# Kernel optimization log

Measured on AMD Instinct MI355X. Metric: run time of the kernel, lower is better.

The kernel has to match this reference:

```python
import jax, jax.numpy as jnp
from jax import lax
import numpy as np

N, D, H, ENT = 32768, 16, 128, 50000


def setup_inputs() -> dict:
    key = jax.random.key(0)
    ks = jax.random.split(key, 10)
    s = 0.05  # weight scale to keep tanh/sigmoid in active range
    return {
        "ent_table": jax.random.normal(ks[0], (ENT, H), jnp.float32) * s,
        "op_table": jax.random.normal(ks[1], (5, H), jnp.float32) * s,
        "non_table": jax.random.normal(ks[2], (1, H), jnp.float32) * s,
        "Wm": jax.random.normal(ks[3], (H, 3 * H), jnp.float32) * s,
        "bm": jnp.zeros((H,), jnp.float32),
        "Wg": jax.random.normal(ks[4], (H, 3 * H), jnp.float32) * s,
        "bg": jnp.zeros((H,), jnp.float32),
        "ops_idx": jax.random.randint(ks[5], (N, D), 0, 4, jnp.int32),
        "ents_idx": jax.random.randint(ks[6], (N, D + 1), 0, ENT, jnp.int32),
        "left_idx": jax.random.randint(ks[7], (N,), 0, ENT, jnp.int32),
    }


def reference(ent_table, op_table, non_table, Wm, bm, Wg, bg, ops_idx, ents_idx, left_idx):
    # Merge module (dropout in eval mode = identity):
    #   tanh(Linear([node, t1, t2])) * sigmoid(Linear_g([node, t1, t2]))
    def merge(node, t1, t2):
        x = jnp.concatenate([node, t1, t2], axis=-1)  # [N, 3H]
        return jnp.tanh(x @ Wm.T + bm) * jax.nn.sigmoid(x @ Wg.T + bg)

    op_e = op_table[ops_idx]        # [N, D, H]
    ent_e = ent_table[ents_idx]     # [N, D+1, H]

    # Right-leaning prefix tree: acc starts at deepest entity, merge upward.
    acc0 = ent_e[:, -1]             # [N, H]
    # scan over depth, from innermost (i = D-1) to outermost (i = 0)
    xs = (jnp.flip(op_e, axis=1).transpose(1, 0, 2),          # [D, N, H]
          jnp.flip(ent_e[:, :-1], axis=1).transpose(1, 0, 2))  # [D, N, H]

    def step(acc, inp):
        o, e = inp
        return merge(o, e, acc), None

    acc, _ = lax.scan(step, acc0, xs)

    eq_e = jnp.broadcast_to(op_table[4], acc.shape)  # '=' embedding, [N, H]
    left_e = ent_table[left_idx]                     # [N, H]
    score = merge(eq_e, left_e, acc)                 # [N, H]

    # all_score = cat(per-formula scores, non_embed)  -> [N+1, H]
    return jnp.concatenate([score, non_table], axis=0)
```

## Files before the change

kernel.cpp:

```cpp
#include <hip/hip_runtime.h>
#include <hip/hip_bf16.h>

#define NROWS 32768
#define HH 128
#define ENTN 50000

typedef _Float16 f16x8 __attribute__((ext_vector_type(8)));
typedef __fp16 fp16x2 __attribute__((ext_vector_type(2)));
typedef float f32x4 __attribute__((ext_vector_type(4)));

#define OFF_PEB 0
#define OFF_EB  25600000
#define OFF_WF  38400000
#define OFF_PEF (OFF_WF + 65536)
#define OFF_PO  (OFF_PEF + 65536)

#define KM 2.8853901f
#define KG (-1.4426950f)
#define RSTR 272
#define HALF (32 * RSTR)

#if defined(__has_builtin)
#if __has_builtin(__builtin_amdgcn_exp2f)
#define FEXP2(x) __builtin_amdgcn_exp2f(x)
#endif
#endif
#ifndef FEXP2
__device__ __forceinline__ float __fexp2_asm(float x) {
    float r; asm("v_exp_f32 %0, %1" : "=v"(r) : "v"(x)); return r;
}
#define FEXP2(x) __fexp2_asm(x)
#endif

__device__ __forceinline__ unsigned pk2(float a, float b) {
    fp16x2 h = __builtin_amdgcn_cvt_pkrtz(a, b);
    unsigned u; __builtin_memcpy(&u, &h, 4); return u;
}
__device__ __forceinline__ float h2f(unsigned short s) {
    _Float16 h; __builtin_memcpy(&h, &s, 2); return (float)h;
}

__global__ void prep_kernel(const float* __restrict__ ent_table,
                            const float* __restrict__ op_table,
                            const float* __restrict__ non_table,
                            const float* __restrict__ Wm, const float* __restrict__ bm,
                            const float* __restrict__ Wg, const float* __restrict__ bg,
                            char* __restrict__ ws, float* __restrict__ out) {
    int idx = blockIdx.x * blockDim.x + threadIdx.x;
    if (idx < 800000) {
        _Float16* EB = (_Float16*)(ws + OFF_EB);
        int base = idx * 8;
        const float4* s = (const float4*)(ent_table + base);
        float4 v0 = s[0], v1 = s[1];
        float xv[8] = {v0.x, v0.y, v0.z, v0.w, v1.x, v1.y, v1.z, v1.w};
        _Float16 h8[8];
        #pragma unroll
        for (int j = 0; j < 8; ++j) h8[j] = (_Float16)xv[j];
        *(f16x8*)(EB + base) = *(f16x8*)h8;
    } else if (idx < 832768) {
        int e = idx - 800000;
        int jj = e & 7, l = (e >> 3) & 63, kt = (e >> 9) & 3, jb = e >> 11;
        int j = jb * 16 + (l & 15);
        int c = j >> 1, p = j & 1;
        int k = kt * 32 + (l >> 4) * 8 + jj;
        const float* Wrow = p ? (Wg + (size_t)c * 384) : (Wm + (size_t)c * 384);
        ((_Float16*)(ws + OFF_WF))[e] = (_Float16)Wrow[256 + k];
    } else if (idx < 865536) {
        int e = idx - 832768;
        int jj = e & 7, l = (e >> 3) & 63, kt = (e >> 9) & 3, jb = e >> 11;
        int j = jb * 16 + (l & 15);
        int c = j >> 1, p = j & 1;
        int k = kt * 32 + (l >> 4) * 8 + jj;
        const float* Wrow = p ? (Wg + (size_t)c * 384) : (Wm + (size_t)c * 384);
        ((_Float16*)(ws + OFF_PEF))[e] = (_Float16)Wrow[128 + k];
    } else if (idx < 866816) {
        int e = idx - 865536;
        int o = e >> 8, jj = e & 255;
        int c = jj >> 1, p = jj & 1;
        const float* Wrow = p ? (Wg + (size_t)c * 384) : (Wm + (size_t)c * 384);
        float s = p ? bg[c] : bm[c];
        for (int i = 0; i < 128; ++i) s += op_table[o * HH + i] * Wrow[i];
        s *= (p ? KG : KM);
        ((float*)(ws + OFF_PO))[o * 260 + (c >> 1) * 4 + 2 * (c & 1) + p] = s;
    } else if (idx < 866944) {
        int j = idx - 866816;
        out[(size_t)NROWS * HH + j] = non_table[j];
    }
}

__global__ __launch_bounds__(256, 4)
void pe_kernel(char* __restrict__ ws) {
    const char* EBc = ws + OFF_EB;
    const f16x8* PEF = (const f16x8*)(ws + OFF_PEF);
    unsigned* PEB = (unsigned*)(ws + OFF_PEB);
    int tid = threadIdx.x, w = tid >> 6, l = tid & 63, lr = l & 15, lg = (l >> 4) & 3;
    int e0 = blockIdx.x * 32;

    f16x8 WB[4][4];
    #pragma unroll
    for (int u = 0; u < 4; ++u)
        #pragma unroll
        for (int kt = 0; kt < 4; ++kt)
            WB[u][kt] = PEF[((4 * w + u) * 4 + kt) * 64 + l];

    f32x4 C[2][4];
    #pragma unroll
    for (int rt = 0; rt < 2; ++rt)
        #pragma unroll
        for (int u = 0; u < 4; ++u) C[rt][u] = (f32x4){0.f, 0.f, 0.f, 0.f};

    #pragma unroll
    for (int kt = 0; kt < 4; ++kt) {
        #pragma unroll
        for (int rt = 0; rt < 2; ++rt) {
            int e = e0 + rt * 16 + lr;
            if (e >= ENTN) e = ENTN - 1;
            f16x8 A = *(const f16x8*)(EBc + (size_t)e * 256 + kt * 64 + lg * 16);
            #pragma unroll
            for (int u = 0; u < 4; ++u)
                C[rt][u] = __builtin_amdgcn_mfma_f32_16x16x32_f16(WB[u][kt], A, C[rt][u], 0, 0, 0);
        }
    }
    #pragma unroll
    for (int rt = 0; rt < 2; ++rt) {
        int e = e0 + rt * 16 + lr;
        if (e < ENTN) {
            #pragma unroll
            for (int u = 0; u < 4; ++u) {
                uint2 st;
                st.x = pk2(C[rt][u][0] * KM, C[rt][u][1] * KG);
                st.y = pk2(C[rt][u][2] * KM, C[rt][u][3] * KG);
                *(uint2*)(PEB + (size_t)e * HH + (4 * w + u) * 8 + 2 * lg) = st;
            }
        }
    }
}

__global__ __launch_bounds__(1024, 8)
void chain_kernel(const float* __restrict__ ent_table,
                  const int* __restrict__ ops_idx,
                  const int* __restrict__ ents_idx,
                  const int* __restrict__ left_idx,
                  const char* __restrict__ ws, float* __restrict__ out) {
    __shared__ char Abuf[2 * HALF];
    __shared__ unsigned eo[32 * 17];
    __shared__ float po_s[5 * 260];

    const char* PEBc = ws + OFF_PEB;
    const f16x8* WF2p = (const f16x8*)(ws + OFF_WF);
    const float* POg = (const float*)(ws + OFF_PO);

    int tid = threadIdx.x;
    int jb = tid >> 6, l = tid & 63, lr = l & 15, lg = (l >> 4) & 3;
    int row0 = blockIdx.x * 32;
    int c1 = jb * 8 + 2 * lg;

    if (tid < 544) {
        int r = tid / 17, t = tid - r * 17;
        unsigned e, o;
        if (t < 16) {
            e = ents_idx[(row0 + r) * 17 + 15 - t];
            o = ops_idx[(row0 + r) * 16 + 15 - t];
        } else {
            e = left_idx[row0 + r];
            o = 4;
        }
        eo[tid] = (e << 9) | o;
    }
    for (int i = tid; i < 1300; i += 1024) po_s[i] = POg[i];

    f16x8 WH[4];
    #pragma unroll
    for (int kt = 0; kt < 4; ++kt)
        WH[kt] = WF2p[(jb * 4 + kt) * 64 + l];

    {
        int r = tid >> 5, sub = tid & 31;
        int e = ents_idx[(row0 + r) * 17 + 16];
        float4 v = *(const float4*)(ent_table + (size_t)e * HH + sub * 4);
        uint2 d;
        d.x = pk2(v.x, v.y);
        d.y = pk2(v.z, v.w);
        *(uint2*)(Abuf + r * RSTR + sub * 8) = d;
    }
    __syncthreads();

    int rb = lr * RSTR + lg * 16;
    int wb = lr * RSTR + jb * 16 + 4 * lg;
    const char* pebBase = PEBc + c1 * 4;
    const float* poBase = po_s + (4 * jb + lg) * 4;
    const unsigned* eoB = eo + lr * 17;

    const f32x4 K4 = (f32x4){KM, KG, KM, KG};

    unsigned va = eoB[0], vb = eoB[272];
    uint2 pea = *(const uint2*)(pebBase + (va & 0xFFFFFE00u));
    uint2 peb = *(const uint2*)(pebBase + (vb & 0xFFFFFE00u));

#define DO_STEP(T, RD, WR, FINAL)                                               \
    {                                                                           \
        uint2 npea, npeb; unsigned nva = 0, nvb = 0;                            \
        if (!(FINAL)) {                                                         \
            nva = eoB[(T) + 1];                                                 \
            nvb = eoB[272 + (T) + 1];                                           \
            npea = *(const uint2*)(pebBase + (nva & 0xFFFFFE00u));              \
            npeb = *(const uint2*)(pebBase + (nvb & 0xFFFFFE00u));              \
        }                                                                       \
        f32x4 poa = *(const f32x4*)(poBase + (va & 7u) * 260);                  \
        f32x4 pob = *(const f32x4*)(poBase + (vb & 7u) * 260);                  \
        f32x4 C0 = (f32x4){0.f, 0.f, 0.f, 0.f};                                 \
        f32x4 C1 = (f32x4){0.f, 0.f, 0.f, 0.f};                                 \
        _Pragma("unroll")                                                       \
        for (int kt = 0; kt < 4; ++kt) {                                        \
            f16x8 A0 = *(const f16x8*)(Abuf + rb + (RD) + kt * 64);             \
            f16x8 A1 = *(const f16x8*)(Abuf + rb + (RD) + 16 * RSTR + kt * 64); \
            C0 = __builtin_amdgcn_mfma_f32_16x16x32_f16(WH[kt], A0, C0, 0, 0, 0); \
            C1 = __builtin_amdgcn_mfma_f32_16x16x32_f16(WH[kt], A1, C1, 0, 0, 0); \
        }                                                                       \
        _Pragma("unroll")                                                       \
        for (int rt = 0; rt < 2; ++rt) {                                        \
            uint2 pe = rt ? peb : pea;                                          \
            f32x4 po = rt ? pob : poa;                                          \
            f32x4 z = rt ? C1 : C0;                                             \
            f32x4 pef;                                                          \
            pef[0] = h2f((unsigned short)pe.x);                                 \
            pef[1] = h2f((unsigned short)(pe.x >> 16));                         \
            pef[2] = h2f((unsigned short)pe.y);                                 \
            pef[3] = h2f((unsigned short)(pe.y >> 16));                         \
            f32x4 s4 = pef + po;                                                \
            f32x4 a = z * K4 + s4;                                              \
            f32x4 ev;                                                           \
            ev[0] = FEXP2(a[0]); ev[1] = FEXP2(a[1]);                           \
            ev[2] = FEXP2(a[2]); ev[3] = FEXP2(a[3]);                           \
            f32x4 p1 = ev + 1.0f;                                               \
            float r1 = (ev[0] - 1.f) * __builtin_amdgcn_rcpf(p1[0] * p1[1]);    \
            float r2 = (ev[2] - 1.f) * __builtin_amdgcn_rcpf(p1[2] * p1[3]);    \
            if (FINAL) {                                                        \
                float2 o2 = make_float2(r1, r2);                                \
                *(float2*)(out + (size_t)(row0 + rt * 16 + lr) * HH + c1) = o2; \
            } else {                                                            \
                *(unsigned*)(Abuf + wb + (WR) + rt * 16 * RSTR) = pk2(r1, r2);  \
            }                                                                   \
        }                                                                       \
        __syncthreads();                                                        \
        if (!(FINAL)) { pea = npea; peb = npeb; va = nva; vb = nvb; }           \
    }

    for (int tb = 0; tb < 8; ++tb) {
        int t0 = 2 * tb;
        DO_STEP(t0, 0, HALF, 0)
        DO_STEP(t0 + 1, HALF, 0, 0)
    }
    DO_STEP(16, 0, HALF, 1)
#undef DO_STEP
}

extern "C" void kernel_launch(void* const* d_in, const int* in_sizes, int n_in,
                              void* d_out, int out_size, void* d_ws, size_t ws_size,
                              hipStream_t stream) {
    const float* ent_table = (const float*)d_in[0];
    const float* op_table  = (const float*)d_in[1];
    const float* non_table = (const float*)d_in[2];
    const float* Wm        = (const float*)d_in[3];
    const float* bm        = (const float*)d_in[4];
    const float* Wg        = (const float*)d_in[5];
    const float* bg        = (const float*)d_in[6];
    const int* ops_idx     = (const int*)d_in[7];
    const int* ents_idx    = (const int*)d_in[8];
    const int* left_idx    = (const int*)d_in[9];
    float* out = (float*)d_out;
    char* ws = (char*)d_ws;

    prep_kernel<<<3387, 256, 0, stream>>>(ent_table, op_table, non_table,
                                          Wm, bm, Wg, bg, ws, out);
    pe_kernel<<<1563, 256, 0, stream>>>(ws);
    chain_kernel<<<NROWS / 32, 1024, 0, stream>>>(ent_table, ops_idx, ents_idx,
                                                  left_idx, ws, out);
}
```

Measured before the change: 107.0 us.

## Switch chain kernel to 32x32x16 MFMA with 512 threads and C-preloaded biases

The recurrent chain kernel now uses 32x32x16 MFMA tiles over all 32 rows per wave, so each block runs 512 threads instead of 1024. The per-entity and per-op pre-activations are stored as packed fp16 in an MFMA-accumulator-friendly layout, added in half precision, and used as the initial accumulator. The KM/KG scaling is folded into the weights so the epilogue needs no multiply. This cuts per-step MFMA and epilogue instruction counts and gathers fewer, wider loads, at the cost of extra fp16 rounding of the bias sums and fewer waves per block.

```diff
diff --git a/kernel.cpp b/kernel.cpp
--- a/kernel.cpp
+++ b/kernel.cpp
@@ -1,5 +1,6 @@
 #include <hip/hip_runtime.h>
 #include <hip/hip_bf16.h>
+#include <hip/hip_fp16.h>
 
 #define NROWS 32768
 #define HH 128
@@ -8,12 +9,13 @@
 typedef _Float16 f16x8 __attribute__((ext_vector_type(8)));
 typedef __fp16 fp16x2 __attribute__((ext_vector_type(2)));
 typedef float f32x4 __attribute__((ext_vector_type(4)));
+typedef float f32x16 __attribute__((ext_vector_type(16)));
 
 #define OFF_PEB 0
 #define OFF_EB  25600000
 #define OFF_WF  38400000
 #define OFF_PEF (OFF_WF + 65536)
-#define OFF_PO  (OFF_PEF + 65536)
+#define OFF_POPK (OFF_PEF + 65536)
 
 #define KM 2.8853901f
 #define KG (-1.4426950f)
@@ -36,8 +38,11 @@
     fp16x2 h = __builtin_amdgcn_cvt_pkrtz(a, b);
     unsigned u; __builtin_memcpy(&u, &h, 4); return u;
 }
-__device__ __forceinline__ float h2f(unsigned short s) {
-    _Float16 h; __builtin_memcpy(&h, &s, 2); return (float)h;
+__device__ __forceinline__ unsigned pk2rtn(float a, float b) {
+    _Float16 lo = (_Float16)a, hi = (_Float16)b;
+    unsigned short ul, uh;
+    __builtin_memcpy(&ul, &lo, 2); __builtin_memcpy(&uh, &hi, 2);
+    return (unsigned)ul | ((unsigned)uh << 16);
 }
 
 __global__ void prep_kernel(const float* __restrict__ ent_table,
@@ -59,12 +64,12 @@
         *(f16x8*)(EB + base) = *(f16x8*)h8;
     } else if (idx < 832768) {
         int e = idx - 800000;
-        int jj = e & 7, l = (e >> 3) & 63, kt = (e >> 9) & 3, jb = e >> 11;
-        int j = jb * 16 + (l & 15);
+        int jj = e & 7, l = (e >> 3) & 63, kt = (e >> 9) & 7, jb = e >> 12;
+        int j = jb * 32 + (l & 31);
         int c = j >> 1, p = j & 1;
-        int k = kt * 32 + (l >> 4) * 8 + jj;
+        int k = kt * 16 + (l >> 5) * 8 + jj;
         const float* Wrow = p ? (Wg + (size_t)c * 384) : (Wm + (size_t)c * 384);
-        ((_Float16*)(ws + OFF_WF))[e] = (_Float16)Wrow[256 + k];
+        ((_Float16*)(ws + OFF_WF))[e] = (_Float16)(Wrow[256 + k] * (p ? KG : KM));
     } else if (idx < 865536) {
         int e = idx - 832768;
         int jj = e & 7, l = (e >> 3) & 63, kt = (e >> 9) & 3, jb = e >> 11;
@@ -73,17 +78,22 @@
         int k = kt * 32 + (l >> 4) * 8 + jj;
         const float* Wrow = p ? (Wg + (size_t)c * 384) : (Wm + (size_t)c * 384);
         ((_Float16*)(ws + OFF_PEF))[e] = (_Float16)Wrow[128 + k];
-    } else if (idx < 866816) {
-        int e = idx - 865536;
-        int o = e >> 8, jj = e & 255;
-        int c = jj >> 1, p = jj & 1;
-        const float* Wrow = p ? (Wg + (size_t)c * 384) : (Wm + (size_t)c * 384);
-        float s = p ? bg[c] : bm[c];
-        for (int i = 0; i < 128; ++i) s += op_table[o * HH + i] * Wrow[i];
-        s *= (p ? KG : KM);
-        ((float*)(ws + OFF_PO))[o * 260 + (c >> 1) * 4 + 2 * (c & 1) + p] = s;
-    } else if (idx < 866944) {
-        int j = idx - 866816;
+    } else if (idx < 866176) {
+        int t2 = idx - 865536;
+        int pr = t2 & 1, q = (t2 >> 1) & 3, h = (t2 >> 3) & 1, jb = (t2 >> 4) & 7, o = t2 >> 7;
+        int j0 = jb * 32 + 8 * q + 4 * h + 2 * pr;
+        int c = j0 >> 1;
+        float sm = bm[c], sg = bg[c];
+        const float* Wrm = Wm + (size_t)c * 384;
+        const float* Wrg = Wg + (size_t)c * 384;
+        for (int i = 0; i < 128; ++i) {
+            float ov = op_table[o * HH + i];
+            sm += ov * Wrm[i];
+            sg += ov * Wrg[i];
+        }
+        ((unsigned*)(ws + OFF_POPK))[t2] = pk2rtn(sm * KM, sg * KG);
+    } else if (idx < 866304) {
+        int j = idx - 866176;
         out[(size_t)NROWS * HH + j] = non_table[j];
     }
 }
@@ -92,7 +102,7 @@
 void pe_kernel(char* __restrict__ ws) {
     const char* EBc = ws + OFF_EB;
     const f16x8* PEF = (const f16x8*)(ws + OFF_PEF);
-    unsigned* PEB = (unsigned*)(ws + OFF_PEB);
+    char* PEB = ws + OFF_PEB;
     int tid = threadIdx.x, w = tid >> 6, l = tid & 63, lr = l & 15, lg = (l >> 4) & 3;
     int e0 = blockIdx.x * 32;
 
@@ -127,123 +137,126 @@
         if (e < ENTN) {
             #pragma unroll
             for (int u = 0; u < 4; ++u) {
+                int c = (4 * w + u) * 8 + 2 * lg;
+                int jb2 = c >> 4, rem = c & 15;
+                int q = rem >> 2, h2 = (rem >> 1) & 1;
                 uint2 st;
                 st.x = pk2(C[rt][u][0] * KM, C[rt][u][1] * KG);
                 st.y = pk2(C[rt][u][2] * KM, C[rt][u][3] * KG);
-                *(uint2*)(PEB + (size_t)e * HH + (4 * w + u) * 8 + 2 * lg) = st;
+                *(uint2*)(PEB + (size_t)e * 512 + jb2 * 64 + h2 * 32 + q * 8) = st;
             }
         }
     }
 }
 
-__global__ __launch_bounds__(1024, 8)
+__global__ __launch_bounds__(512, 4)
 void chain_kernel(const float* __restrict__ ent_table,
                   const int* __restrict__ ops_idx,
                   const int* __restrict__ ents_idx,
                   const int* __restrict__ left_idx,
                   const char* __restrict__ ws, float* __restrict__ out) {
     __shared__ char Abuf[2 * HALF];
-    __shared__ unsigned eo[32 * 17];
-    __shared__ float po_s[5 * 260];
+    __shared__ unsigned eo[17 * 32];
+    __shared__ unsigned popk[640];
 
     const char* PEBc = ws + OFF_PEB;
-    const f16x8* WF2p = (const f16x8*)(ws + OFF_WF);
-    const float* POg = (const float*)(ws + OFF_PO);
+    const f16x8* WFp = (const f16x8*)(ws + OFF_WF);
+    const unsigned* POPKg = (const unsigned*)(ws + OFF_POPK);
 
     int tid = threadIdx.x;
-    int jb = tid >> 6, l = tid & 63, lr = l & 15, lg = (l >> 4) & 3;
+    int jb = tid >> 6, l = tid & 63, r = l & 31, h = l >> 5;
     int row0 = blockIdx.x * 32;
-    int c1 = jb * 8 + 2 * lg;
-
-    if (tid < 544) {
-        int r = tid / 17, t = tid - r * 17;
+
+    for (int i = tid; i < 544; i += 512) {
+        int t = i >> 5, rr = i & 31;
         unsigned e, o;
         if (t < 16) {
-            e = ents_idx[(row0 + r) * 17 + 15 - t];
-            o = ops_idx[(row0 + r) * 16 + 15 - t];
+            e = ents_idx[(row0 + rr) * 17 + 15 - t];
+            o = ops_idx[(row0 + rr) * 16 + 15 - t];
         } else {
-            e = left_idx[row0 + r];
+            e = left_idx[row0 + rr];
             o = 4;
         }
-        eo[tid] = (e << 9) | o;
-    }
-    for (int i = tid; i < 1300; i += 1024) po_s[i] = POg[i];
-
-    f16x8 WH[4];
-    #pragma unroll
-    for (int kt = 0; kt < 4; ++kt)
-        WH[kt] = WF2p[(jb * 4 + kt) * 64 + l];
+        eo[i] = (e << 9) | o;
+    }
+    for (int i = tid; i < 640; i += 512) popk[i] = POPKg[i];
+
+    f16x8 WH[8];
+    #pragma unroll
+    for (int kt = 0; kt < 8; ++kt)
+        WH[kt] = WFp[(jb * 8 + kt) * 64 + l];
 
     {
-        int r = tid >> 5, sub = tid & 31;
-        int e = ents_idx[(row0 + r) * 17 + 16];
-        float4 v = *(const float4*)(ent_table + (size_t)e * HH + sub * 4);
-        uint2 d;
-        d.x = pk2(v.x, v.y);
-        d.y = pk2(v.z, v.w);
-        *(uint2*)(Abuf + r * RSTR + sub * 8) = d;
+        int rr = tid >> 4, sub = tid & 15;
+        int e = ents_idx[(row0 + rr) * 17 + 16];
+        const float4* src = (const float4*)(ent_table + (size_t)e * HH + sub * 8);
+        float4 v0 = src[0], v1 = src[1];
+        uint4 d;
+        d.x = pk2(v0.x, v0.y); d.y = pk2(v0.z, v0.w);
+        d.z = pk2(v1.x, v1.y); d.w = pk2(v1.z, v1.w);
+        *(uint4*)(Abuf + rr * RSTR + sub * 16) = d;
     }
     __syncthreads();
 
-    int rb = lr * RSTR + lg * 16;
-    int wb = lr * RSTR + jb * 16 + 4 * lg;
-    const char* pebBase = PEBc + c1 * 4;
-    const float* poBase = po_s + (4 * jb + lg) * 4;
-    const unsigned* eoB = eo + lr * 17;
-
-    const f32x4 K4 = (f32x4){KM, KG, KM, KG};
-
-    unsigned va = eoB[0], vb = eoB[272];
-    uint2 pea = *(const uint2*)(pebBase + (va & 0xFFFFFE00u));
-    uint2 peb = *(const uint2*)(pebBase + (vb & 0xFFFFFE00u));
+    int rb = r * RSTR + h * 16;
+    int wb = r * RSTR + jb * 32 + h * 4;
+    const char* pebBase = PEBc + jb * 64 + h * 32;
+    const char* popkB = (const char*)popk + jb * 64 + h * 32;
+    const unsigned* eoB = eo + r;
+
+    unsigned va = eoB[0];
+    uint4 pa0 = *(const uint4*)(pebBase + (va & 0xFFFFFE00u));
+    uint4 pa1 = *(const uint4*)(pebBase + (va & 0xFFFFFE00u) + 16);
 
 #define DO_STEP(T, RD, WR, FINAL)                                               \
     {                                                                           \
-        uint2 npea, npeb; unsigned nva = 0, nvb = 0;                            \
+        uint4 npa0, npa1; unsigned nva = 0;                                     \
         if (!(FINAL)) {                                                         \
-            nva = eoB[(T) + 1];                                                 \
-            nvb = eoB[272 + (T) + 1];                                           \
-            npea = *(const uint2*)(pebBase + (nva & 0xFFFFFE00u));              \
-            npeb = *(const uint2*)(pebBase + (nvb & 0xFFFFFE00u));              \
+            nva = eoB[((T) + 1) * 32];                                          \
+            npa0 = *(const uint4*)(pebBase + (nva & 0xFFFFFE00u));              \
+            npa1 = *(const uint4*)(pebBase + (nva & 0xFFFFFE00u) + 16);         \
         }                                                                       \
-        f32x4 poa = *(const f32x4*)(poBase + (va & 7u) * 260);                  \
-        f32x4 pob = *(const f32x4*)(poBase + (vb & 7u) * 260);                  \
-        f32x4 C0 = (f32x4){0.f, 0.f, 0.f, 0.f};                                 \
-        f32x4 C1 = (f32x4){0.f, 0.f, 0.f, 0.f};                                 \
+        const char* pq = popkB + (va & 7u) * 512;                               \
+        uint4 po0 = *(const uint4*)(pq);                                        \
+        uint4 po1 = *(const uint4*)(pq + 16);                                   \
+        unsigned pe_u[8] = {pa0.x, pa0.y, pa0.z, pa0.w, pa1.x, pa1.y, pa1.z, pa1.w}; \
+        unsigned po_u[8] = {po0.x, po0.y, po0.z, po0.w, po1.x, po1.y, po1.z, po1.w}; \
+        f32x16 C;                                                               \
         _Pragma("unroll")                                                       \
-        for (int kt = 0; kt < 4; ++kt) {                                        \
-            f16x8 A0 = *(const f16x8*)(Abuf + rb + (RD) + kt * 64);             \
-            f16x8 A1 = *(const f16x8*)(Abuf + rb + (RD) + 16 * RSTR + kt * 64); \
-            C0 = __builtin_amdgcn_mfma_f32_16x16x32_f16(WH[kt], A0, C0, 0, 0, 0); \
-            C1 = __builtin_amdgcn_mfma_f32_16x16x32_f16(WH[kt], A1, C1, 0, 0, 0); \
+        for (int q = 0; q < 4; ++q)                                             \
+            _Pragma("unroll")                                                   \
+            for (int pr = 0; pr < 2; ++pr) {                                    \
+                int u = q * 2 + pr;                                             \
+                __half2 sa = *(const __half2*)&pe_u[u];                         \
+                __half2 sb = *(const __half2*)&po_u[u];                         \
+                __half2 s = __hadd2(sa, sb);                                    \
+                C[4 * q + 2 * pr] = __low2float(s);                             \
+                C[4 * q + 2 * pr + 1] = __high2float(s);                        \
+            }                                                                   \
+        _Pragma("unroll")                                                       \
+        for (int kt = 0; kt < 8; ++kt) {                                        \
+            f16x8 A = *(const f16x8*)(Abuf + rb + (RD) + kt * 32);              \
+            C = __builtin_amdgcn_mfma_f32_32x32x16_f16(WH[kt], A, C, 0, 0, 0);  \
         }                                                                       \
         _Pragma("unroll")                                                       \
-        for (int rt = 0; rt < 2; ++rt) {                                        \
-            uint2 pe = rt ? peb : pea;                                          \
-            f32x4 po = rt ? pob : poa;                                          \
-            f32x4 z = rt ? C1 : C0;                                             \
-            f32x4 pef;                                                          \
-            pef[0] = h2f((unsigned short)pe.x);                                 \
-            pef[1] = h2f((unsigned short)(pe.x >> 16));                         \
-            pef[2] = h2f((unsigned short)pe.y);                                 \
-            pef[3] = h2f((unsigned short)(pe.y >> 16));                         \
-            f32x4 s4 = pef + po;                                                \
-            f32x4 a = z * K4 + s4;                                              \
-            f32x4 ev;                                                           \
-            ev[0] = FEXP2(a[0]); ev[1] = FEXP2(a[1]);                           \
-            ev[2] = FEXP2(a[2]); ev[3] = FEXP2(a[3]);                           \
-            f32x4 p1 = ev + 1.0f;                                               \
-            float r1 = (ev[0] - 1.f) * __builtin_amdgcn_rcpf(p1[0] * p1[1]);    \
-            float r2 = (ev[2] - 1.f) * __builtin_amdgcn_rcpf(p1[2] * p1[3]);    \
+        for (int q = 0; q < 4; ++q) {                                           \
+            float ov[2];                                                        \
+            _Pragma("unroll")                                                   \
+            for (int pr = 0; pr < 2; ++pr) {                                    \
+                float m = C[4 * q + 2 * pr];                                    \
+                float g = C[4 * q + 2 * pr + 1];                                \
+                float em = FEXP2(m), eg = FEXP2(g);                             \
+                ov[pr] = (em - 1.f) * __builtin_amdgcn_rcpf((em + 1.f) * (1.f + eg)); \
+            }                                                                   \
             if (FINAL) {                                                        \
-                float2 o2 = make_float2(r1, r2);                                \
-                *(float2*)(out + (size_t)(row0 + rt * 16 + lr) * HH + c1) = o2; \
+                *(float2*)(out + (size_t)(row0 + r) * HH + jb * 16 + 4 * q + 2 * h) \
+                    = make_float2(ov[0], ov[1]);                                \
             } else {                                                            \
-                *(unsigned*)(Abuf + wb + (WR) + rt * 16 * RSTR) = pk2(r1, r2);  \
+                *(unsigned*)(Abuf + wb + (WR) + q * 8) = pk2(ov[0], ov[1]);     \
             }                                                                   \
         }                                                                       \
         __syncthreads();                                                        \
-        if (!(FINAL)) { pea = npea; peb = npeb; va = nva; vb = nvb; }           \
+        if (!(FINAL)) { pa0 = npa0; pa1 = npa1; va = nva; }                     \
     }
 
     for (int tb = 0; tb < 8; ++tb) {
@@ -271,9 +284,9 @@
     float* out = (float*)d_out;
     char* ws = (char*)d_ws;
 
-    prep_kernel<<<3387, 256, 0, stream>>>(ent_table, op_table, non_table,
+    prep_kernel<<<3384, 256, 0, stream>>>(ent_table, op_table, non_table,
                                           Wm, bm, Wg, bg, ws, out);
     pe_kernel<<<1563, 256, 0, stream>>>(ws);
-    chain_kernel<<<NROWS / 32, 1024, 0, stream>>>(ent_table, ops_idx, ents_idx,
-                                                  left_idx, ws, out);
-}
+    chain_kernel<<<NROWS / 32, 512, 0, stream>>>(ent_table, ops_idx, ents_idx,
+                                                 left_idx, ws, out);
+}
```

Measured after the change: 101.7 us. -4.9%, faster.
